# Kernel optimization log

Measured on AMD Instinct MI355X. Metric: run time of the kernel, lower is better.

Reference implementation:

```python
import jax, jax.numpy as jnp
import numpy as np

T, KBLK, EMB, B = 2048, 64, 512, 4


def _make_coords(t, k):
    # head1: for each j, cols = block_start(j) + arange(j % k + 1)  (block-causal local)
    j = np.arange(t)
    cnt1 = (j % k) + 1
    rows1 = np.repeat(j, cnt1)
    off1 = np.arange(cnt1.sum()) - np.repeat(np.cumsum(cnt1) - cnt1, cnt1)
    cols1 = (rows1 // k) * k + off1
    # head2: for each block start c, rows = arange(c, t), col = c  (strided block-start)
    starts = np.arange(t // k) * k
    cnt2 = t - starts
    base = np.repeat(starts, cnt2)
    off2 = np.arange(cnt2.sum()) - np.repeat(np.cumsum(cnt2) - cnt2, cnt2)
    rows2, cols2 = base + off2, base
    c1 = np.stack([rows1, cols1], 1).astype(np.int32)
    c2 = np.stack([rows2, cols2], 1).astype(np.int32)
    return c1, c2


def setup_inputs() -> dict:
    key = jax.random.key(0)
    ks = jax.random.split(key, 6)
    s = 1.0 / float(np.sqrt(EMB))
    c1, c2 = _make_coords(T, KBLK)
    return {
        "x": jax.random.normal(ks[0], (B, T, EMB), jnp.float32),
        "Wk": jax.random.normal(ks[1], (EMB, EMB), jnp.float32) * s,
        "bk": jnp.zeros((EMB,), jnp.float32),
        "Wq": jax.random.normal(ks[2], (EMB, EMB), jnp.float32) * s,
        "bq": jnp.zeros((EMB,), jnp.float32),
        "Wv": jax.random.normal(ks[3], (EMB, EMB), jnp.float32) * s,
        "bv": jnp.zeros((EMB,), jnp.float32),
        "Wu": jax.random.normal(ks[4], (EMB, 2 * EMB), jnp.float32) * s,
        "bu": jnp.zeros((EMB,), jnp.float32),
        "coords1": jnp.asarray(c1),
        "coords2": jnp.asarray(c2),
    }


def _sparse_head(Kt, Qt, Vt, coords):
    rows, cols = coords[:, 0], coords[:, 1]
    # dot[b,p] = (K @ Q^T)[b, rows[p], cols[p]] = K[b,rows[p],:] . Q[b,cols[p],:]
    dot = jnp.einsum('bpe,bpe->bp', Kt[:, rows], Qt[:, cols])
    # sparse.batchmm: out[b,r] = sum_{p: rows[p]=r} dot[b,p] * V[b, cols[p]]
    out = jnp.zeros_like(Vt).at[:, rows].add(dot[..., None] * Vt[:, cols])
    return out


def reference(x, Wk, bk, Wq, bq, Wv, bv, Wu, bu, coords1, coords2):
    Kt = x @ Wk.T + bk
    Qt = x @ Wq.T + bq
    Vt = x @ Wv.T + bv
    h1 = _sparse_head(Kt, Qt, Vt, coords1)
    h2 = _sparse_head(Kt, Qt, Vt, coords2)
    comb = jnp.concatenate([h1, h2], axis=-1)  # [B, T, 2*EMB]
    return comb @ Wu.T + bu
```

## Files before the change

kernel.cpp:

```cpp
#include <hip/hip_runtime.h>


typedef unsigned short u16;
typedef __attribute__((ext_vector_type(8))) short short8;
typedef __attribute__((ext_vector_type(4))) float f32x4;

constexpr int TDIM  = 2048;
constexpr int EMB_D = 512;
constexpr int BB    = 4;
constexpr int NBLK  = 32;
constexpr int LDK   = 2048;

__device__ __forceinline__ u16 f2b(float f) {
    unsigned u = __float_as_uint(f);
    unsigned r = (u + 0x7FFFu + ((u >> 16) & 1u)) >> 16;
    return (u16)r;
}

__global__ __launch_bounds__(256) void prep_k(
    const float* __restrict__ x, const float* __restrict__ Wk, const float* __restrict__ Wq,
    const float* __restrict__ Wv, const float* __restrict__ Wu,
    const float* __restrict__ bk, const float* __restrict__ bq, const float* __restrict__ bv,
    u16* __restrict__ xb, u16* __restrict__ wcat, u16* __restrict__ wvtb,
    u16* __restrict__ wub, float* __restrict__ biascat)
{
    const int bid = blockIdx.x, tid = threadIdx.x;
    if (bid < 5120) {
        const float* src; u16* dst; int base;
        if (bid < 4096)      { src = x;  dst = xb;            base = bid * 1024; }
        else if (bid < 4352) { src = Wk; dst = wcat;          base = (bid - 4096) * 1024; }
        else if (bid < 4608) { src = Wq; dst = wcat + 262144; base = (bid - 4352) * 1024; }
        else                 { src = Wu; dst = wub;           base = (bid - 4608) * 1024; }
        const int idx = base + tid * 4;
        float4 v = *(const float4*)(src + idx);
        ushort4 o = { f2b(v.x), f2b(v.y), f2b(v.z), f2b(v.w) };
        *(ushort4*)(dst + idx) = o;
    } else if (bid < 5184) {
        __shared__ float T[64][65];
        const int t = bid - 5120;
        const int j0 = (t >> 3) * 64, k0 = (t & 7) * 64;
        const int rr = tid >> 4, c4 = (tid & 15) * 4;
        #pragma unroll
        for (int it = 0; it < 4; ++it) {
            const int j = rr + it * 16;
            float4 v = *(const float4*)(Wv + (size_t)(j0 + j) * 512 + k0 + c4);
            T[c4+0][j] = v.x; T[c4+1][j] = v.y; T[c4+2][j] = v.z; T[c4+3][j] = v.w;
        }
        __syncthreads();
        #pragma unroll
        for (int it = 0; it < 4; ++it) {
            const int k = rr + it * 16;
            ushort4 o = { f2b(T[k][c4+0]), f2b(T[k][c4+1]), f2b(T[k][c4+2]), f2b(T[k][c4+3]) };
            *(ushort4*)(wvtb + (size_t)(k0 + k) * 512 + j0 + c4) = o;
        }
    } else if (bid < 5200) {
        const int o = (bid - 5184) * 64 + (tid >> 2);
        const int p = tid & 3;
        const int n = o & 511, half = o >> 9;
        const float* wr = Wu + (size_t)n * 1024 + half * 512 + p * 128;
        const float* br = bv + p * 128;
        float s = 0.f;
        #pragma unroll
        for (int j = 0; j < 128; j += 4) {
            float4 a = *(const float4*)(wr + j);
            float4 b = *(const float4*)(br + j);
            s += a.x*b.x + a.y*b.y + a.z*b.z + a.w*b.w;
        }
        s += __shfl_xor(s, 1);
        s += __shfl_xor(s, 2);
        if (p == 0) biascat[1024 + o] = s;
    } else {
        const int idx = tid * 4;
        float4 v = (idx < 512) ? *(const float4*)(bk + idx)
                               : *(const float4*)(bq + idx - 512);
        *(float4*)(biascat + idx) = v;
    }
}

__global__ __launch_bounds__(256) void wc_gemm_k(
    const u16* __restrict__ wub, const u16* __restrict__ wvtb, u16* __restrict__ wcat)
{
    __shared__ u16 As[128 * 32];
    __shared__ u16 Bs[128 * 32];
    const int bm = blockIdx.x * 128;
    const int bn = blockIdx.y * 128;
    const int tid  = threadIdx.x;
    const int wid  = tid >> 6;
    const int lane = tid & 63;
    const int l15  = lane & 15;
    const int quad = lane >> 4;
    const int wm = (wid & 1) * 64;
    const int wn = (wid >> 1) * 64;

    f32x4 acc[4][4] = {};

    const int srow  = tid >> 2;
    const int skoff = (tid & 3) * 8;
    const int m0 = bm + srow, m1 = bm + 64 + srow;
    const u16* Ag0 = wub + (size_t)(m0 & 511) * 1024 + (m0 >> 9) * 512 + skoff;
    const u16* Ag1 = wub + (size_t)(m1 & 511) * 1024 + (m1 >> 9) * 512 + skoff;
    const u16* Bg  = wvtb + (size_t)(bn + srow) * 512 + skoff;
    char* AsBase = (char*)As + wid * 1024;
    char* BsBase = (char*)Bs + wid * 1024;

    for (int k0 = 0; k0 < 512; k0 += 32) {
        __syncthreads();
        __builtin_amdgcn_global_load_lds(
            (const __attribute__((address_space(1))) void*)(Ag0 + k0),
            (__attribute__((address_space(3))) void*)AsBase, 16, 0, 0);
        __builtin_amdgcn_global_load_lds(
            (const __attribute__((address_space(1))) void*)(Ag1 + k0),
            (__attribute__((address_space(3))) void*)(AsBase + 4096), 16, 0, 0);
        __builtin_amdgcn_global_load_lds(
            (const __attribute__((address_space(1))) void*)(Bg + k0),
            (__attribute__((address_space(3))) void*)BsBase, 16, 0, 0);
        __builtin_amdgcn_global_load_lds(
            (const __attribute__((address_space(1))) void*)(Bg + (size_t)64 * 512 + k0),
            (__attribute__((address_space(3))) void*)(BsBase + 4096), 16, 0, 0);
        __syncthreads();

        short8 a[4], b[4];
        #pragma unroll
        for (int i = 0; i < 4; ++i)
            a[i] = *(const short8*)((const short*)As + (wm + 16 * i + l15) * 32 + quad * 8);
        #pragma unroll
        for (int j = 0; j < 4; ++j)
            b[j] = *(const short8*)((const short*)Bs + (wn + 16 * j + l15) * 32 + quad * 8);
        #pragma unroll
        for (int i = 0; i < 4; ++i)
            #pragma unroll
            for (int j = 0; j < 4; ++j)
                acc[i][j] = __builtin_amdgcn_mfma_f32_16x16x32_bf16(a[i], b[j], acc[i][j], 0, 0, 0);
    }

    #pragma unroll
    for (int i = 0; i < 4; ++i)
        #pragma unroll
        for (int j = 0; j < 4; ++j) {
            const int col = bn + wn + 16 * j + l15;
            #pragma unroll
            for (int r = 0; r < 4; ++r) {
                const int row = bm + wm + 16 * i + quad * 4 + r;
                wcat[(size_t)(1024 + row) * 512 + col] = f2b(acc[i][j][r]);
            }
        }
}

__global__ __launch_bounds__(256) void kqv_gemm_k(
    const u16* __restrict__ A, const u16* __restrict__ W,
    const float* __restrict__ bias, u16* __restrict__ C)
{
    __shared__ u16 As[128 * 32];
    __shared__ u16 Bs[128 * 32];
    const int bm = blockIdx.x * 128;
    const int bn = blockIdx.y * 128;
    const int tid  = threadIdx.x;
    const int wid  = tid >> 6;
    const int lane = tid & 63;
    const int l15  = lane & 15;
    const int quad = lane >> 4;
    const int wm = (wid & 1) * 64;
    const int wn = (wid >> 1) * 64;

    f32x4 acc[4][4] = {};

    const int srow  = tid >> 2;
    const int skoff = (tid & 3) * 8;
    const u16* Ag = A + (size_t)(bm + srow) * EMB_D + skoff;
    const u16* Wg = W + (size_t)(bn + srow) * EMB_D + skoff;
    char* AsBase = (char*)As + wid * 1024;
    char* BsBase = (char*)Bs + wid * 1024;

    for (int k0 = 0; k0 < EMB_D; k0 += 32) {
        __syncthreads();
        __builtin_amdgcn_global_load_lds(
            (const __attribute__((address_space(1))) void*)(Ag + k0),
            (__attribute__((address_space(3))) void*)AsBase, 16, 0, 0);
        __builtin_amdgcn_global_load_lds(
            (const __attribute__((address_space(1))) void*)(Ag + (size_t)64 * EMB_D + k0),
            (__attribute__((address_space(3))) void*)(AsBase + 4096), 16, 0, 0);
        __builtin_amdgcn_global_load_lds(
            (const __attribute__((address_space(1))) void*)(Wg + k0),
            (__attribute__((address_space(3))) void*)BsBase, 16, 0, 0);
        __builtin_amdgcn_global_load_lds(
            (const __attribute__((address_space(1))) void*)(Wg + (size_t)64 * EMB_D + k0),
            (__attribute__((address_space(3))) void*)(BsBase + 4096), 16, 0, 0);
        __syncthreads();

        short8 a[4], b[4];
        #pragma unroll
        for (int i = 0; i < 4; ++i)
            a[i] = *(const short8*)((const short*)As + (wm + 16 * i + l15) * 32 + quad * 8);
        #pragma unroll
        for (int j = 0; j < 4; ++j)
            b[j] = *(const short8*)((const short*)Bs + (wn + 16 * j + l15) * 32 + quad * 8);
        #pragma unroll
        for (int i = 0; i < 4; ++i)
            #pragma unroll
            for (int j = 0; j < 4; ++j)
                acc[i][j] = __builtin_amdgcn_mfma_f32_16x16x32_bf16(a[i], b[j], acc[i][j], 0, 0, 0);
    }

    #pragma unroll
    for (int i = 0; i < 4; ++i) {
        #pragma unroll
        for (int j = 0; j < 4; ++j) {
            const int col = bn + wn + 16 * j + l15;
            const float bvv = bias[col];
            #pragma unroll
            for (int r = 0; r < 4; ++r) {
                const int row = bm + wm + 16 * i + quad * 4 + r;
                C[(size_t)row * LDK + col] = f2b(acc[i][j][r] + bvv);
            }
        }
    }
}

__global__ __launch_bounds__(256) void heads_k(
    const u16* __restrict__ KQV, const float* __restrict__ bu, float* __restrict__ out)
{
    __shared__ u16 smA[64 * 104];
    __shared__ u16 smVT[128 * 104];
    __shared__ u16 pK[2][64 * 32];
    __shared__ u16 pQ[2][64 * 32];
    __shared__ u16 pQs[2][32 * 32];

    const int blk = blockIdx.x, b = blockIdx.y;
    const int e0 = blockIdx.z * 128;
    const int tid = threadIdx.x;
    const int wid = tid >> 6, lane = tid & 63;
    const int l15 = lane & 15, quad = lane >> 4;
    const size_t row0 = (size_t)b * TDIM + (size_t)blk * 64;
    const size_t brow = (size_t)b * TDIM;
    const int srow_base = 16 * wid + quad * 4;

    #pragma unroll
    for (int it = 0; it < 4; ++it) {
        const int id = tid + 256 * it;
        const int c  = id & 63;
        const int eo = (id >> 6) * 8;
        short8 v = *(const short8*)(KQV + (row0 + c) * (size_t)LDK + 1024 + e0 + eo);
        #pragma unroll
        for (int i = 0; i < 8; ++i) smVT[(eo + i) * 104 + c] = (u16)v[i];
    }
    #pragma unroll
    for (int it = 0; it < 2; ++it) {
        const int id = tid + 256 * it;
        const int m  = id & 31;
        const int eo = (id >> 5) * 8;
        short8 v = *(const short8*)(KQV + (brow + 64 * m) * (size_t)LDK + 1536 + e0 + eo);
        #pragma unroll
        for (int i = 0; i < 8; ++i) smVT[(eo + i) * 104 + 64 + m] = (u16)v[i];
    }

    f32x4 s1[4] = {}; f32x4 s2[2] = {};
    const int srow  = tid >> 2;
    const int skoff = (tid & 3) * 8;
    const int qsrow = srow & 31;
    const int qsp   = tid >> 7;
    const u16* Kg  = KQV + (row0 + srow) * (size_t)LDK + skoff;
    const u16* Qg  = KQV + (row0 + srow) * (size_t)LDK + 512 + skoff;
    const u16* Qsg = KQV + (brow + (size_t)64 * qsrow) * (size_t)LDK + 512 + qsp * 32 + skoff;
    char* dK  = (char*)pK  + wid * 1024;
    char* dQ  = (char*)pQ  + wid * 1024;
    char* dQs = (char*)pQs + wid * 1024;

    for (int k0 = 0; k0 < 512; k0 += 64) {
        __syncthreads();
        __builtin_amdgcn_global_load_lds(
            (const __attribute__((address_space(1))) void*)(Kg + k0),
            (__attribute__((address_space(3))) void*)dK, 16, 0, 0);
        __builtin_amdgcn_global_load_lds(
            (const __attribute__((address_space(1))) void*)(Kg + k0 + 32),
            (__attribute__((address_space(3))) void*)(dK + 4096), 16, 0, 0);
        __builtin_amdgcn_global_load_lds(
            (const __attribute__((address_space(1))) void*)(Qg + k0),
            (__attribute__((address_space(3))) void*)dQ, 16, 0, 0);
        __builtin_amdgcn_global_load_lds(
            (const __attribute__((address_space(1))) void*)(Qg + k0 + 32),
            (__attribute__((address_space(3))) void*)(dQ + 4096), 16, 0, 0);
        __builtin_amdgcn_global_load_lds(
            (const __attribute__((address_space(1))) void*)(Qsg + k0),
            (__attribute__((address_space(3))) void*)dQs, 16, 0, 0);
        __syncthreads();

        short8 a0 = *(const short8*)(pK[0] + (16 * wid + l15) * 32 + quad * 8);
        short8 a1 = *(const short8*)(pK[1] + (16 * wid + l15) * 32 + quad * 8);
        #pragma unroll
        for (int j = 0; j < 4; ++j) {
            short8 b0 = *(const short8*)(pQ[0] + (16 * j + l15) * 32 + quad * 8);
            short8 b1 = *(const short8*)(pQ[1] + (16 * j + l15) * 32 + quad * 8);
            s1[j] = __builtin_amdgcn_mfma_f32_16x16x32_bf16(a0, b0, s1[j], 0, 0, 0);
            s1[j] = __builtin_amdgcn_mfma_f32_16x16x32_bf16(a1, b1, s1[j], 0, 0, 0);
        }
        #pragma unroll
        for (int j = 0; j < 2; ++j) {
            short8 b0 = *(const short8*)(pQs[0] + (16 * j + l15) * 32 + quad * 8);
            short8 b1 = *(const short8*)(pQs[1] + (16 * j + l15) * 32 + quad * 8);
            s2[j] = __builtin_amdgcn_mfma_f32_16x16x32_bf16(a0, b0, s2[j], 0, 0, 0);
            s2[j] = __builtin_amdgcn_mfma_f32_16x16x32_bf16(a1, b1, s2[j], 0, 0, 0);
        }
    }

    #pragma unroll
    for (int j = 0; j < 4; ++j)
        #pragma unroll
        for (int r = 0; r < 4; ++r) {
            const int rr = srow_base + r;
            const int cc = 16 * j + l15;
            smA[rr * 104 + cc] = f2b((cc <= rr) ? s1[j][r] : 0.0f);
        }
    #pragma unroll
    for (int j = 0; j < 2; ++j)
        #pragma unroll
        for (int r = 0; r < 4; ++r) {
            const int m  = 16 * j + l15;
            const int rr = srow_base + r;
            smA[rr * 104 + 64 + m] = f2b((m <= blk) ? s2[j][r] : 0.0f);
        }
    __syncthreads();

    f32x4 o[8] = {};
    const u16* arow = smA + (16 * wid + l15) * 104;
    #pragma unroll
    for (int ks = 0; ks < 3; ++ks) {
        short8 as = *(const short8*)(arow + 32 * ks + quad * 8);
        #pragma unroll
        for (int nt = 0; nt < 8; ++nt) {
            short8 bs = *(const short8*)(smVT + (16 * nt + l15) * 104 + 32 * ks + quad * 8);
            o[nt] = __builtin_amdgcn_mfma_f32_16x16x32_bf16(as, bs, o[nt], 0, 0, 0);
        }
    }
    #pragma unroll
    for (int nt = 0; nt < 8; ++nt) {
        const int col = e0 + 16 * nt + l15;
        const float bvv = bu[col];
        #pragma unroll
        for (int r = 0; r < 4; ++r)
            out[(row0 + srow_base + r) * (size_t)EMB_D + col] = o[nt][r] + bvv;
    }
}

extern "C" void kernel_launch(void* const* d_in, const int* in_sizes, int n_in,
                              void* d_out, int out_size, void* d_ws, size_t ws_size,
                              hipStream_t stream)
{
    const float* x  = (const float*)d_in[0];
    const float* Wk = (const float*)d_in[1];
    const float* bk = (const float*)d_in[2];
    const float* Wq = (const float*)d_in[3];
    const float* bq = (const float*)d_in[4];
    const float* Wv = (const float*)d_in[5];
    const float* bv = (const float*)d_in[6];
    const float* Wu = (const float*)d_in[7];
    const float* bu = (const float*)d_in[8];
    float* out = (float*)d_out;

    char* w = (char*)d_ws;
    u16*   KQV     = (u16*)  (w + ((size_t)0  << 20));
    u16*   xb      = (u16*)  (w + ((size_t)32 << 20));
    u16*   wcat    = (u16*)  (w + ((size_t)40 << 20));
    u16*   wvtb    = (u16*)  (w + ((size_t)42 << 20));
    u16*   wub     = (u16*)  (w + ((size_t)43 << 20));
    float* biascat = (float*)(w + ((size_t)44 << 20));

    dim3 blk(256);
    hipLaunchKernelGGL(prep_k, dim3(5201), blk, 0, stream,
                       x, Wk, Wq, Wv, Wu, bk, bq, bv, xb, wcat, wvtb, wub, biascat);
    hipLaunchKernelGGL(wc_gemm_k, dim3(8, 4), blk, 0, stream, wub, wvtb, wcat);
    hipLaunchKernelGGL(kqv_gemm_k, dim3(64, 16), blk, 0, stream, xb, wcat, biascat, KQV);
    hipLaunchKernelGGL(heads_k, dim3(NBLK, BB, 4), blk, 0, stream, KQV, bu, out);
}
```

Baseline: 149.0 us.

## Rewrite KQV GEMM as 256x256 tile, double-buffered, swizzled LDS pipeline

The KQV projection GEMM moves from 128x128 tiles with 256 threads and a single LDS buffer to 256x256 tiles with 512 threads. It uses a double-buffered 128KB LDS ring with XOR-swizzled layout, interleaves async global-to-LDS loads with MFMA phases, raises wave priority during MFMA, and remaps block IDs for L2 locality. The aim is to hide global load latency, cut LDS bank conflicts and raise data reuse per tile. In exchange the schedule is complex and hand-tuned with explicit waitcnt/barriers. It also launches only 256 blocks, which risks correctness hazards and lower occupancy.

```diff
diff --git a/kernel.cpp b/kernel.cpp
--- a/kernel.cpp
+++ b/kernel.cpp
@@ -146,75 +146,153 @@
         }
 }
 
-__global__ __launch_bounds__(256) void kqv_gemm_k(
+template<int MH, int KK>
+__device__ __forceinline__ void mm16(const short8 (&a)[4], const short8 (&b)[2][4],
+                                     f32x4 (&acc)[8][4])
+{
+    #pragma unroll
+    for (int f = 0; f < 4; ++f)
+        #pragma unroll
+        for (int g = 0; g < 4; ++g)
+            acc[MH * 4 + f][g] = __builtin_amdgcn_mfma_f32_16x16x32_bf16(
+                a[f], b[KK][g], acc[MH * 4 + f][g], 0, 0, 0);
+}
+
+template<int SLOT, int MH>
+__device__ __forceinline__ void lda4(short8 (&a)[4], const u16* sm, int arow, int koff)
+{
+    #pragma unroll
+    for (int f = 0; f < 4; ++f)
+        a[f] = *(const short8*)(sm + SLOT * 32768 + (arow + MH * 64 + f * 16) * 64 + koff);
+}
+
+template<int SLOT>
+__device__ __forceinline__ void ldb4(short8 (&bk)[4], const u16* sm, int brow, int koff)
+{
+    #pragma unroll
+    for (int g = 0; g < 4; ++g)
+        bk[g] = *(const short8*)(sm + SLOT * 32768 + 16384 + (brow + g * 16) * 64 + koff);
+}
+
+#define STA(S, CI, T) __builtin_amdgcn_global_load_lds( \
+    (const __attribute__((address_space(1))) void*)(Ag + (size_t)(CI) * 32768 + (T) * 64), \
+    (__attribute__((address_space(3))) void*)(sm + (S) * 32768 + (CI) * 4096 + wid * 512), 16, 0, 0)
+#define STB(S, CI, T) __builtin_amdgcn_global_load_lds( \
+    (const __attribute__((address_space(1))) void*)(Bg + (size_t)(CI) * 32768 + (T) * 64), \
+    (__attribute__((address_space(3))) void*)(sm + (S) * 32768 + 16384 + (CI) * 4096 + wid * 512), 16, 0, 0)
+#define KBAR()  __builtin_amdgcn_s_barrier()
+#define KPRIO(P) __builtin_amdgcn_s_setprio(P)
+#define LGKM0() do { asm volatile("s_waitcnt lgkmcnt(0)" ::: "memory"); \
+                     __builtin_amdgcn_sched_barrier(0); } while (0)
+#define VMC4()  asm volatile("s_waitcnt vmcnt(4)" ::: "memory")
+#define VMC0()  asm volatile("s_waitcnt vmcnt(0)" ::: "memory")
+
+__global__ __launch_bounds__(512, 2) void kqv_gemm_k(
     const u16* __restrict__ A, const u16* __restrict__ W,
     const float* __restrict__ bias, u16* __restrict__ C)
 {
-    __shared__ u16 As[128 * 32];
-    __shared__ u16 Bs[128 * 32];
-    const int bm = blockIdx.x * 128;
-    const int bn = blockIdx.y * 128;
+    __shared__ u16 sm[65536];
+
+    const int bid = blockIdx.x;
+    const int wg  = (bid & 7) * 32 + (bid >> 3);
+    const int bm  = (wg & 31) * 256;
+    const int bn  = (wg >> 5) * 256;
     const int tid  = threadIdx.x;
     const int wid  = tid >> 6;
     const int lane = tid & 63;
     const int l15  = lane & 15;
     const int quad = lane >> 4;
-    const int wm = (wid & 1) * 64;
-    const int wn = (wid >> 1) * 64;
-
-    f32x4 acc[4][4] = {};
-
-    const int srow  = tid >> 2;
-    const int skoff = (tid & 3) * 8;
-    const u16* Ag = A + (size_t)(bm + srow) * EMB_D + skoff;
-    const u16* Wg = W + (size_t)(bn + srow) * EMB_D + skoff;
-    char* AsBase = (char*)As + wid * 1024;
-    char* BsBase = (char*)Bs + wid * 1024;
-
-    for (int k0 = 0; k0 < EMB_D; k0 += 32) {
-        __syncthreads();
-        __builtin_amdgcn_global_load_lds(
-            (const __attribute__((address_space(1))) void*)(Ag + k0),
-            (__attribute__((address_space(3))) void*)AsBase, 16, 0, 0);
-        __builtin_amdgcn_global_load_lds(
-            (const __attribute__((address_space(1))) void*)(Ag + (size_t)64 * EMB_D + k0),
-            (__attribute__((address_space(3))) void*)(AsBase + 4096), 16, 0, 0);
-        __builtin_amdgcn_global_load_lds(
-            (const __attribute__((address_space(1))) void*)(Wg + k0),
-            (__attribute__((address_space(3))) void*)BsBase, 16, 0, 0);
-        __builtin_amdgcn_global_load_lds(
-            (const __attribute__((address_space(1))) void*)(Wg + (size_t)64 * EMB_D + k0),
-            (__attribute__((address_space(3))) void*)(BsBase + 4096), 16, 0, 0);
-        __syncthreads();
-
-        short8 a[4], b[4];
-        #pragma unroll
-        for (int i = 0; i < 4; ++i)
-            a[i] = *(const short8*)((const short*)As + (wm + 16 * i + l15) * 32 + quad * 8);
-        #pragma unroll
-        for (int j = 0; j < 4; ++j)
-            b[j] = *(const short8*)((const short*)Bs + (wn + 16 * j + l15) * 32 + quad * 8);
-        #pragma unroll
-        for (int i = 0; i < 4; ++i)
-            #pragma unroll
-            for (int j = 0; j < 4; ++j)
-                acc[i][j] = __builtin_amdgcn_mfma_f32_16x16x32_bf16(a[i], b[j], acc[i][j], 0, 0, 0);
-    }
-
-    #pragma unroll
-    for (int i = 0; i < 4; ++i) {
-        #pragma unroll
-        for (int j = 0; j < 4; ++j) {
-            const int col = bn + wn + 16 * j + l15;
+    const int wm = wid >> 2;
+    const int wn = wid & 3;
+
+    const int stgrow = wid * 8 + (lane >> 3);
+    const int stgk   = ((lane & 7) ^ ((lane >> 3) & 7)) << 3;
+    const u16* Ag = A + (size_t)(bm + stgrow) * 512 + stgk;
+    const u16* Bg = W + (size_t)(bn + stgrow) * 512 + stgk;
+
+    const int r7     = l15 & 7;
+    const int arow   = wm * 128 + l15;
+    const int brow   = wn * 64 + l15;
+    const int off_k0 = ((quad ^ r7) << 3);
+    const int off_k1 = (((4 | quad) ^ r7) << 3);
+
+    f32x4 acc[8][4] = {};
+    short8 a[4], b[2][4];
+
+    STA(0,0,0); STA(0,2,0); STB(0,0,0); STB(0,1,0);
+    STB(0,2,0); STB(0,3,0); STA(0,1,0); STA(0,3,0);
+    STA(1,0,1); STA(1,2,1); STB(1,0,1); STB(1,1,1);
+    VMC4(); KBAR();
+
+    for (int it = 0; it < 3; ++it) {
+        const int t = 2 * it;
+        ldb4<0>(b[0], sm, brow, off_k0); lda4<0,0>(a, sm, arow, off_k0);
+        STB(1,2,t+1); STB(1,3,t+1);
+        KBAR(); LGKM0(); KPRIO(1); mm16<0,0>(a, b, acc); KPRIO(0); KBAR();
+        ldb4<0>(b[1], sm, brow, off_k1); lda4<0,0>(a, sm, arow, off_k1);
+        STA(1,1,t+1); STA(1,3,t+1);
+        KBAR(); LGKM0(); KPRIO(1); mm16<0,1>(a, b, acc); KPRIO(0); KBAR();
+        lda4<0,1>(a, sm, arow, off_k0);
+        STA(0,0,t+2); STA(0,2,t+2);
+        KBAR(); LGKM0(); KPRIO(1); mm16<1,0>(a, b, acc); KPRIO(0); KBAR();
+        lda4<0,1>(a, sm, arow, off_k1);
+        STB(0,0,t+2); STB(0,1,t+2);
+        KBAR(); LGKM0(); KPRIO(1); mm16<1,1>(a, b, acc); KPRIO(0); VMC4(); KBAR();
+        ldb4<1>(b[0], sm, brow, off_k0); lda4<1,0>(a, sm, arow, off_k0);
+        STB(0,2,t+2); STB(0,3,t+2);
+        KBAR(); LGKM0(); KPRIO(1); mm16<0,0>(a, b, acc); KPRIO(0); KBAR();
+        ldb4<1>(b[1], sm, brow, off_k1); lda4<1,0>(a, sm, arow, off_k1);
+        STA(0,1,t+2); STA(0,3,t+2);
+        KBAR(); LGKM0(); KPRIO(1); mm16<0,1>(a, b, acc); KPRIO(0); KBAR();
+        lda4<1,1>(a, sm, arow, off_k0);
+        STA(1,0,t+3); STA(1,2,t+3);
+        KBAR(); LGKM0(); KPRIO(1); mm16<1,0>(a, b, acc); KPRIO(0); KBAR();
+        lda4<1,1>(a, sm, arow, off_k1);
+        STB(1,0,t+3); STB(1,1,t+3);
+        KBAR(); LGKM0(); KPRIO(1); mm16<1,1>(a, b, acc); KPRIO(0); VMC4(); KBAR();
+    }
+
+    ldb4<0>(b[0], sm, brow, off_k0); lda4<0,0>(a, sm, arow, off_k0);
+    STB(1,2,7); STB(1,3,7);
+    KBAR(); LGKM0(); KPRIO(1); mm16<0,0>(a, b, acc); KPRIO(0); KBAR();
+    ldb4<0>(b[1], sm, brow, off_k1); lda4<0,0>(a, sm, arow, off_k1);
+    STA(1,1,7); STA(1,3,7);
+    KBAR(); LGKM0(); KPRIO(1); mm16<0,1>(a, b, acc); KPRIO(0); KBAR();
+    lda4<0,1>(a, sm, arow, off_k0);
+    KBAR(); LGKM0(); KPRIO(1); mm16<1,0>(a, b, acc); KPRIO(0); KBAR();
+    lda4<0,1>(a, sm, arow, off_k1);
+    KBAR(); LGKM0(); KPRIO(1); mm16<1,1>(a, b, acc); KPRIO(0); VMC0(); KBAR();
+    ldb4<1>(b[0], sm, brow, off_k0); lda4<1,0>(a, sm, arow, off_k0);
+    KBAR(); LGKM0(); KPRIO(1); mm16<0,0>(a, b, acc); KPRIO(0); KBAR();
+    ldb4<1>(b[1], sm, brow, off_k1); lda4<1,0>(a, sm, arow, off_k1);
+    KBAR(); LGKM0(); KPRIO(1); mm16<0,1>(a, b, acc); KPRIO(0); KBAR();
+    lda4<1,1>(a, sm, arow, off_k0);
+    KBAR(); LGKM0(); KPRIO(1); mm16<1,0>(a, b, acc); KPRIO(0); KBAR();
+    lda4<1,1>(a, sm, arow, off_k1);
+    KBAR(); LGKM0(); KPRIO(1); mm16<1,1>(a, b, acc); KPRIO(0);
+
+    #pragma unroll
+    for (int mf = 0; mf < 8; ++mf) {
+        #pragma unroll
+        for (int g = 0; g < 4; ++g) {
+            const int col = bn + wn * 64 + g * 16 + l15;
             const float bvv = bias[col];
             #pragma unroll
             for (int r = 0; r < 4; ++r) {
-                const int row = bm + wm + 16 * i + quad * 4 + r;
-                C[(size_t)row * LDK + col] = f2b(acc[i][j][r] + bvv);
+                const int row = bm + wm * 128 + mf * 16 + quad * 4 + r;
+                C[(size_t)row * LDK + col] = f2b(acc[mf][g][r] + bvv);
             }
         }
     }
 }
+
+#undef STA
+#undef STB
+#undef KBAR
+#undef KPRIO
+#undef LGKM0
+#undef VMC4
+#undef VMC0
 
 __global__ __launch_bounds__(256) void heads_k(
     const u16* __restrict__ KQV, const float* __restrict__ bu, float* __restrict__ out)
@@ -364,10 +442,9 @@
     u16*   wub     = (u16*)  (w + ((size_t)43 << 20));
     float* biascat = (float*)(w + ((size_t)44 << 20));
 
-    dim3 blk(256);
-    hipLaunchKernelGGL(prep_k, dim3(5201), blk, 0, stream,
+    hipLaunchKernelGGL(prep_k, dim3(5201), dim3(256), 0, stream,
                        x, Wk, Wq, Wv, Wu, bk, bq, bv, xb, wcat, wvtb, wub, biascat);
-    hipLaunchKernelGGL(wc_gemm_k, dim3(8, 4), blk, 0, stream, wub, wvtb, wcat);
-    hipLaunchKernelGGL(kqv_gemm_k, dim3(64, 16), blk, 0, stream, xb, wcat, biascat, KQV);
-    hipLaunchKernelGGL(heads_k, dim3(NBLK, BB, 4), blk, 0, stream, KQV, bu, out);
-}
+    hipLaunchKernelGGL(wc_gemm_k, dim3(8, 4), dim3(256), 0, stream, wub, wvtb, wcat);
+    hipLaunchKernelGGL(kqv_gemm_k, dim3(256), dim3(512), 0, stream, xb, wcat, biascat, KQV);
+    hipLaunchKernelGGL(heads_k, dim3(NBLK, BB, 4), dim3(256), 0, stream, KQV, bu, out);
+}
```

New measurement: 144.4 us. -3.1%, faster.
